# Optimization experiments

Hardware: AMD Instinct MI355X
Metric: run time of the kernel (lower is better)

Reference implementation:

```python
import jax, jax.numpy as jnp
import numpy as np

WS = 8          # window / grid size
HEADS = 4


def rel_pos_index(wh, ww):
    # Swin-style pairwise relative position index, [wh*ww, wh*ww]
    coords = np.stack(np.meshgrid(np.arange(wh), np.arange(ww), indexing='ij'))
    cf = coords.reshape(2, -1)
    rel = (cf[:, :, None] - cf[:, None, :]).transpose(1, 2, 0)
    rel[:, :, 0] += wh - 1
    rel[:, :, 1] += ww - 1
    rel[:, :, 0] *= 2 * ww - 1
    return rel.sum(-1)

REL_IDX = rel_pos_index(WS, WS)  # static, [N, N]


def setup_inputs() -> dict:
    key = jax.random.key(0)
    ks = jax.random.split(key, 8)
    B, C, H, W = 4, 128, 256, 256
    return {
        'x': jax.random.normal(ks[0], (B, C, H, W), jnp.float32),
        'w_qkv': jax.random.normal(ks[1], (C, 3 * C), jnp.float32) * 0.02,
        'b_qkv': jnp.zeros((3 * C,), jnp.float32),
        'w_proj': jax.random.normal(ks[2], (C, C), jnp.float32) * 0.02,
        'b_proj': jnp.zeros((C,), jnp.float32),
        'rpb_table': jax.random.normal(ks[3], ((2 * WS - 1) ** 2, HEADS), jnp.float32) * 0.02,
        'cf_w1': jax.random.normal(ks[4], (C, C), jnp.float32) * 0.02,
        'cf_w2': jax.random.normal(ks[5], (C, C), jnp.float32) * 0.02,
    }


def _window_partition(x):
    # [B,C,H,W] -> [B*nw, ws*ws, C], contiguous windows
    B, C, H, W = x.shape
    x = x.reshape(B, C, H // WS, WS, W // WS, WS)
    return x.transpose(0, 2, 4, 3, 5, 1).reshape(-1, WS * WS, C)


def _window_reverse(xw, B, C, H, W):
    x = xw.reshape(B, H // WS, W // WS, WS, WS, C)
    return x.transpose(0, 5, 1, 3, 2, 4).reshape(B, C, H, W)


def _grid_partition(x):
    # [B,C,H,W] -> [B*ng, gs*gs, C], strided (grid) windows
    B, C, H, W = x.shape
    x = x.reshape(B, C, WS, H // WS, WS, W // WS)
    return x.transpose(0, 3, 5, 2, 4, 1).reshape(-1, WS * WS, C)


def _grid_reverse(xg, B, C, H, W):
    x = xg.reshape(B, H // WS, W // WS, WS, WS, C)
    return x.transpose(0, 5, 3, 1, 4, 2).reshape(B, C, H, W)


def _rel_attention(xw, w_qkv, b_qkv, w_proj, b_proj, rpb_table):
    # xw: [Bw, N, C]  MaxViT-style relative self-attention
    Bw, N, C = xw.shape
    hd = C // HEADS
    qkv = (xw @ w_qkv + b_qkv).reshape(Bw, N, 3, HEADS, hd)
    q = qkv[:, :, 0].transpose(0, 2, 1, 3)  # [Bw,h,N,d]
    k = qkv[:, :, 1].transpose(0, 2, 1, 3)
    v = qkv[:, :, 2].transpose(0, 2, 1, 3)
    scale = HEADS ** -0.5
    bias = rpb_table[REL_IDX.reshape(-1)].reshape(N, N, HEADS).transpose(2, 0, 1)  # [h,N,N]
    logits = jnp.einsum('bhnd,bhmd->bhnm', q, k) * scale + bias[None]
    attn = jax.nn.softmax(logits, axis=-1)
    out = jnp.einsum('bhnm,bhmd->bhnd', attn, v)
    out = out.transpose(0, 2, 1, 3).reshape(Bw, N, C)
    return out @ w_proj + b_proj


def reference(x, w_qkv, b_qkv, w_proj, b_proj, rpb_table, cf_w1, cf_w2):
    B, C, H, W = x.shape
    # block (window) attention with residual
    xw = _window_partition(x)
    x = x + _window_reverse(_rel_attention(xw, w_qkv, b_qkv, w_proj, b_proj, rpb_table), B, C, H, W)
    # grid attention with residual
    xg = _grid_partition(x)
    x = x + _grid_reverse(_rel_attention(xg, w_qkv, b_qkv, w_proj, b_proj, rpb_table), B, C, H, W)
    # ChannelFocus: sigmoid(MLP(avgpool) + MLP(maxpool)) channel gate
    avg = x.mean(axis=(2, 3))  # [B,C]
    mx = x.max(axis=(2, 3))    # [B,C]
    mlp = lambda z: jax.nn.relu(z @ cf_w1) @ cf_w2
    gate = jax.nn.sigmoid(mlp(avg) + mlp(mx))  # [B,C]
    return x * gate[:, :, None, None]
```

## Files before the change

### kernel.cpp

```cpp
#include <hip/hip_runtime.h>
#include <hip/hip_bf16.h>
#include <stdint.h>

typedef __bf16 bf16;
typedef bf16 bf16x8 __attribute__((ext_vector_type(8)));
typedef bf16 bf16x4 __attribute__((ext_vector_type(4)));
typedef float f32x4 __attribute__((ext_vector_type(4)));

#define MFMA16(a, b, c) __builtin_amdgcn_mfma_f32_16x16x32_bf16((a), (b), (c), 0, 0, 0)
#define QKSWZ(n) ((((n) >> 2) & 3) << 3)
#define LGKM0() do { asm volatile("s_waitcnt lgkmcnt(0)" ::: "memory"); \
                     __builtin_amdgcn_sched_barrier(0); } while (0)

__global__ __launch_bounds__(256) void tin_kernel(const float* __restrict__ x,
                                                  bf16* __restrict__ xT)
{
    __shared__ float s[128 * 65];
    const int blk = blockIdx.x;
    const int b = blk >> 10;
    const int px0 = (blk & 1023) * 64;
    const int tid = threadIdx.x;
    {
        int c0 = tid >> 6, pxl = tid & 63;
        const float* src = x + (size_t)b * 8388608 + px0 + pxl;
#pragma unroll
        for (int i = 0; i < 32; ++i) {
            int c = c0 + i * 4;
            s[c * 65 + pxl] = src[(size_t)c * 65536];
        }
    }
    __syncthreads();
    int px = tid >> 2, piece = tid & 3;
    bf16* dstp = xT + ((size_t)b * 65536 + px0 + px) * 128;
#pragma unroll
    for (int k = 0; k < 4; ++k) {
        bf16x8 v8;
        int cb = (k * 4 + piece) * 8;
#pragma unroll
        for (int j = 0; j < 8; ++j) v8[j] = (bf16)s[(cb + j) * 65 + px];
        *(bf16x8*)(dstp + cb) = v8;
    }
}

__global__ void wconv_kernel(const float* __restrict__ w_qkv,
                             const float* __restrict__ w_proj,
                             bf16* __restrict__ wqkvT,
                             bf16* __restrict__ wprojT)
{
    int id = blockIdx.x * 256 + threadIdx.x;
    if (id < 49152) {
        int co = id >> 7, c = id & 127;
        wqkvT[id] = (bf16)w_qkv[c * 384 + co];
    } else {
        int id2 = id - 49152;
        int co = id2 >> 7, c = id2 & 127;
        wprojT[id2] = (bf16)w_proj[c * 128 + co];
    }
}

template<int STAGE>
__global__ __launch_bounds__(256, 3)
void attn_kernel(const bf16* __restrict__ xin, bf16* __restrict__ xout,
                 const bf16* __restrict__ wqkvT, const bf16* __restrict__ wprojT,
                 const float* __restrict__ b_qkv, const float* __restrict__ b_proj,
                 const float* __restrict__ rpb,
                 float* __restrict__ psum, float* __restrict__ pmax)
{
    __shared__ __align__(16) bf16 s_x[8192];
    __shared__ __align__(16) bf16 s_ex[8192];
    __shared__ bf16 s_rpb[904];

    const int tid = threadIdx.x;
    const int lane = tid & 63;
    const int wv = tid >> 6;
    const int lr = lane & 15;
    const int lg = lane >> 4;
    bf16* exq = s_ex + wv * 2048;
    bf16* exv = s_x + wv * 2048;

    const int blk = (blockIdx.x & 7) * 512 + (blockIdx.x >> 3);
    const int b  = blk >> 10;
    const int wr = (blk >> 5) & 31;
    const int wc = blk & 31;

    if constexpr (STAGE == 0) {
        int n = tid >> 2, piece = tid & 3;
        int ph = wr * 8 + (n >> 3), pw = wc * 8 + (n & 7);
        const bf16* src = xin + ((size_t)b * 65536 + (size_t)ph * 256 + pw) * 128;
#pragma unroll
        for (int k = 0; k < 4; ++k) {
            int cc = (k * 4 + piece) * 8;
            bf16x8 v = *(const bf16x8*)(src + cc);
            *(bf16x8*)&s_x[(n * 128 + cc) ^ ((n & 15) << 3)] = v;
        }
    } else {
        const bf16* src = xin + ((size_t)b * 65536 + (size_t)(wr * 32 + wc) * 64) * 128;
#pragma unroll
        for (int k = 0; k < 4; ++k) {
            int g = k * 256 + tid;
            int n = g >> 4, cc = (g & 15) * 8;
            bf16x8 v = *(const bf16x8*)(src + g * 8);
            *(bf16x8*)&s_x[(n * 128 + cc) ^ ((n & 15) << 3)] = v;
        }
    }
    for (int i = tid; i < 900; i += 256) s_rpb[i] = (bf16)rpb[i];

    __syncthreads();

    bf16x8 qb[4];
    {
        f32x4 acc[4][2];
#pragma unroll
        for (int mt = 0; mt < 4; ++mt)
#pragma unroll
            for (int t = 0; t < 2; ++t) acc[mt][t] = (f32x4){0.f, 0.f, 0.f, 0.f};
        bf16x8 wB[2][4];
#pragma unroll
        for (int t = 0; t < 2; ++t) {
            int co = wv * 32 + t * 16 + lr;
            const bf16* rp = wqkvT + co * 128 + lg * 8;
#pragma unroll
            for (int ks = 0; ks < 4; ++ks) wB[t][ks] = *(const bf16x8*)(rp + ks * 32);
        }
#pragma unroll
        for (int ks = 0; ks < 4; ++ks) {
            bf16x8 a[4];
#pragma unroll
            for (int mt = 0; mt < 4; ++mt) {
                int n = mt * 16 + lr;
                a[mt] = *(const bf16x8*)&s_x[(n * 128 + ks * 32 + lg * 8) ^ ((n & 15) << 3)];
            }
#pragma unroll
            for (int mt = 0; mt < 4; ++mt)
#pragma unroll
                for (int t = 0; t < 2; ++t)
                    acc[mt][t] = MFMA16(a[mt], wB[t][ks], acc[mt][t]);
        }
#pragma unroll
        for (int t = 0; t < 2; ++t) {
            float bias = b_qkv[wv * 32 + t * 16 + lr];
            int d = t * 16 + lr;
#pragma unroll
            for (int mt = 0; mt < 4; ++mt) {
                int n0 = mt * 16 + lg * 4;
#pragma unroll
                for (int r = 0; r < 4; ++r) {
                    int n = n0 + r;
                    exq[n * 32 + (d ^ QKSWZ(n))] = (bf16)(acc[mt][t][r] + bias);
                }
            }
        }
        LGKM0();
#pragma unroll
        for (int t = 0; t < 4; ++t) {
            int m = t * 16 + lr;
            qb[t] = *(const bf16x8*)&exq[m * 32 + ((lg * 8) ^ QKSWZ(m))];
        }
        LGKM0();
    }

    {
        f32x4 acc[4][2];
#pragma unroll
        for (int mt = 0; mt < 4; ++mt)
#pragma unroll
            for (int t = 0; t < 2; ++t) acc[mt][t] = (f32x4){0.f, 0.f, 0.f, 0.f};
        bf16x8 wB[2][4];
#pragma unroll
        for (int t = 0; t < 2; ++t) {
            int co = 128 + wv * 32 + t * 16 + lr;
            const bf16* rp = wqkvT + co * 128 + lg * 8;
#pragma unroll
            for (int ks = 0; ks < 4; ++ks) wB[t][ks] = *(const bf16x8*)(rp + ks * 32);
        }
#pragma unroll
        for (int ks = 0; ks < 4; ++ks) {
            bf16x8 a[4];
#pragma unroll
            for (int mt = 0; mt < 4; ++mt) {
                int n = mt * 16 + lr;
                a[mt] = *(const bf16x8*)&s_x[(n * 128 + ks * 32 + lg * 8) ^ ((n & 15) << 3)];
            }
#pragma unroll
            for (int mt = 0; mt < 4; ++mt)
#pragma unroll
                for (int t = 0; t < 2; ++t)
                    acc[mt][t] = MFMA16(a[mt], wB[t][ks], acc[mt][t]);
        }
#pragma unroll
        for (int t = 0; t < 2; ++t) {
            float bias = b_qkv[128 + wv * 32 + t * 16 + lr];
            int d = t * 16 + lr;
#pragma unroll
            for (int mt = 0; mt < 4; ++mt) {
                int n0 = mt * 16 + lg * 4;
#pragma unroll
                for (int r = 0; r < 4; ++r) {
                    int n = n0 + r;
                    exq[n * 32 + (d ^ QKSWZ(n))] = (bf16)(acc[mt][t][r] + bias);
                }
            }
        }
    }

    bf16x4 resr[2][4];
#pragma unroll
    for (int ct = 0; ct < 2; ++ct)
#pragma unroll
        for (int nt = 0; nt < 4; ++nt) {
            int n = nt * 16 + lr;
            int c0 = wv * 32 + ct * 16 + lg * 4;
            resr[ct][nt] = *(const bf16x4*)&s_x[(n * 128 + c0) ^ ((n & 15) << 3)];
        }

    f32x4 accV[4][2];
    {
#pragma unroll
        for (int mt = 0; mt < 4; ++mt)
#pragma unroll
            for (int t = 0; t < 2; ++t) accV[mt][t] = (f32x4){0.f, 0.f, 0.f, 0.f};
        bf16x8 wB[2][4];
#pragma unroll
        for (int t = 0; t < 2; ++t) {
            int co = 256 + wv * 32 + t * 16 + lr;
            const bf16* rp = wqkvT + co * 128 + lg * 8;
#pragma unroll
            for (int ks = 0; ks < 4; ++ks) wB[t][ks] = *(const bf16x8*)(rp + ks * 32);
        }
#pragma unroll
        for (int ks = 0; ks < 4; ++ks) {
            bf16x8 a[4];
#pragma unroll
            for (int mt = 0; mt < 4; ++mt) {
                int n = mt * 16 + lr;
                a[mt] = *(const bf16x8*)&s_x[(n * 128 + ks * 32 + lg * 8) ^ ((n & 15) << 3)];
            }
#pragma unroll
            for (int mt = 0; mt < 4; ++mt)
#pragma unroll
                for (int t = 0; t < 2; ++t)
                    accV[mt][t] = MFMA16(a[mt], wB[t][ks], accV[mt][t]);
        }
    }

    __syncthreads();

#pragma unroll
    for (int t = 0; t < 2; ++t) {
        float bias = b_qkv[256 + wv * 32 + t * 16 + lr];
        int d = t * 16 + lr;
#pragma unroll
        for (int mt = 0; mt < 4; ++mt) {
            bf16x4 v4;
#pragma unroll
            for (int r = 0; r < 4; ++r) v4[r] = (bf16)(accV[mt][t][r] + bias);
            int idx = (d * 64 + mt * 16 + lg * 4) ^ ((d & 7) << 3);
            *(bf16x4*)&exv[idx] = v4;
        }
    }

    f32x4 sacc[4][4];
#pragma unroll
    for (int mt = 0; mt < 4; ++mt)
#pragma unroll
        for (int nt = 0; nt < 4; ++nt) sacc[mt][nt] = (f32x4){0.f, 0.f, 0.f, 0.f};
#pragma unroll
    for (int mt = 0; mt < 4; ++mt) {
        int m = mt * 16 + lr;
        bf16x8 ka = *(const bf16x8*)&exq[m * 32 + ((lg * 8) ^ QKSWZ(m))];
#pragma unroll
        for (int nt = 0; nt < 4; ++nt)
            sacc[mt][nt] = MFMA16(ka, qb[nt], sacc[mt][nt]);
    }

    float inv[4];
#pragma unroll
    for (int nt = 0; nt < 4; ++nt) {
        int n = nt * 16 + lr;
        float mx = -1e30f;
#pragma unroll
        for (int mt = 0; mt < 4; ++mt)
#pragma unroll
            for (int r = 0; r < 4; ++r) {
                int m = mt * 16 + lg * 4 + r;
                int rel = ((n >> 3) - (m >> 3) + 7) * 15 + ((n & 7) - (m & 7) + 7);
                float lgt = sacc[mt][nt][r] * 0.5f + (float)s_rpb[rel * 4 + wv];
                sacc[mt][nt][r] = lgt;
                mx = fmaxf(mx, lgt);
            }
        mx = fmaxf(mx, __shfl_xor(mx, 16));
        mx = fmaxf(mx, __shfl_xor(mx, 32));
        float sum = 0.f;
#pragma unroll
        for (int mt = 0; mt < 4; ++mt)
#pragma unroll
            for (int r = 0; r < 4; ++r) {
                float p = __expf(sacc[mt][nt][r] - mx);
                sacc[mt][nt][r] = p;
                sum += p;
            }
        sum += __shfl_xor(sum, 16);
        sum += __shfl_xor(sum, 32);
        inv[nt] = 1.f / sum;
    }
    LGKM0();

    bf16x8 va[2][2];
#pragma unroll
    for (int dt = 0; dt < 2; ++dt) {
        int d = dt * 16 + lr;
#pragma unroll
        for (int ks = 0; ks < 2; ++ks)
            va[dt][ks] = *(const bf16x8*)&exv[(d * 64 + ks * 32 + lg * 8) ^ ((d & 7) << 3)];
    }

    __syncthreads();

    f32x4 oacc[2][4];
#pragma unroll
    for (int dt = 0; dt < 2; ++dt)
#pragma unroll
        for (int nt = 0; nt < 4; ++nt) oacc[dt][nt] = (f32x4){0.f, 0.f, 0.f, 0.f};
#pragma unroll
    for (int ks = 0; ks < 2; ++ks) {
#pragma unroll
        for (int nt = 0; nt < 4; ++nt) {
            int n = nt * 16 + lr;
#pragma unroll
            for (int mh = 0; mh < 2; ++mh) {
                int mt = ks * 2 + mh;
                bf16x4 v4;
#pragma unroll
                for (int r = 0; r < 4; ++r) v4[r] = (bf16)(sacc[mt][nt][r] * inv[nt]);
                int off = (mh * 16 + lg * 4) ^ ((n & 3) << 3);
                *(bf16x4*)&exq[n * 32 + off] = v4;
            }
        }
        LGKM0();
        bf16x8 pb[4];
#pragma unroll
        for (int nt = 0; nt < 4; ++nt) {
            int n = nt * 16 + lr;
            pb[nt] = *(const bf16x8*)&exq[n * 32 + ((lg * 8) ^ ((n & 3) << 3))];
        }
#pragma unroll
        for (int dt = 0; dt < 2; ++dt)
#pragma unroll
            for (int nt = 0; nt < 4; ++nt)
                oacc[dt][nt] = MFMA16(va[dt][ks], pb[nt], oacc[dt][nt]);
        LGKM0();
    }

#pragma unroll
    for (int dt = 0; dt < 2; ++dt)
#pragma unroll
        for (int nt = 0; nt < 4; ++nt) {
            int n = nt * 16 + lr;
            int c0 = wv * 32 + dt * 16 + lg * 4;
            bf16x4 v4;
#pragma unroll
            for (int r = 0; r < 4; ++r) v4[r] = (bf16)oacc[dt][nt][r];
            int idx = (n * 128 + c0) ^ ((n & 15) << 3);
            *(bf16x4*)&s_x[idx] = v4;
        }

    __syncthreads();

    f32x4 pacc[2][4];
#pragma unroll
    for (int ct = 0; ct < 2; ++ct)
#pragma unroll
        for (int nt = 0; nt < 4; ++nt) pacc[ct][nt] = (f32x4){0.f, 0.f, 0.f, 0.f};
#pragma unroll
    for (int ks = 0; ks < 4; ++ks) {
        bf16x8 wa[2], ab[4];
#pragma unroll
        for (int ct = 0; ct < 2; ++ct) {
            int co = wv * 32 + ct * 16 + lr;
            wa[ct] = *(const bf16x8*)(wprojT + co * 128 + ks * 32 + lg * 8);
        }
#pragma unroll
        for (int nt = 0; nt < 4; ++nt) {
            int n = nt * 16 + lr;
            ab[nt] = *(const bf16x8*)&s_x[(n * 128 + ks * 32 + lg * 8) ^ ((n & 15) << 3)];
        }
#pragma unroll
        for (int ct = 0; ct < 2; ++ct)
#pragma unroll
            for (int nt = 0; nt < 4; ++nt)
                pacc[ct][nt] = MFMA16(wa[ct], ab[nt], pacc[ct][nt]);
    }

    float bp[2][4];
#pragma unroll
    for (int ct = 0; ct < 2; ++ct)
#pragma unroll
        for (int r = 0; r < 4; ++r) bp[ct][r] = b_proj[wv * 32 + ct * 16 + lg * 4 + r];

    float vout[2][4][4];
    float ps[2][4], pm[2][4];
    if constexpr (STAGE == 1) {
#pragma unroll
        for (int ct = 0; ct < 2; ++ct)
#pragma unroll
            for (int r = 0; r < 4; ++r) { ps[ct][r] = 0.f; pm[ct][r] = -1e30f; }
    }
#pragma unroll
    for (int ct = 0; ct < 2; ++ct)
#pragma unroll
        for (int nt = 0; nt < 4; ++nt)
#pragma unroll
            for (int r = 0; r < 4; ++r) {
                float v = (float)resr[ct][nt][r] + bp[ct][r] + pacc[ct][nt][r];
                vout[ct][nt][r] = v;
                if constexpr (STAGE == 1) {
                    ps[ct][r] += v;
                    pm[ct][r] = fmaxf(pm[ct][r], v);
                }
            }

    if constexpr (STAGE == 1) {
        const int w = blk & 1023;
        float* prow_s = psum + (size_t)w * 512 + b * 128;
        float* prow_m = pmax + (size_t)w * 512 + b * 128;
#pragma unroll
        for (int ct = 0; ct < 2; ++ct)
#pragma unroll
            for (int r = 0; r < 4; ++r) {
                float s = ps[ct][r], m = pm[ct][r];
#pragma unroll
                for (int o = 1; o < 16; o <<= 1) {
                    s += __shfl_xor(s, o);
                    m = fmaxf(m, __shfl_xor(m, o));
                }
                if (lr == 0) {
                    int cout = wv * 32 + ct * 16 + lg * 4 + r;
                    prow_s[cout] = s;
                    prow_m[cout] = m;
                }
            }
    }

    __syncthreads();

#pragma unroll
    for (int ct = 0; ct < 2; ++ct)
#pragma unroll
        for (int nt = 0; nt < 4; ++nt) {
            int n = nt * 16 + lr;
            int c0 = wv * 32 + ct * 16 + lg * 4;
            bf16x4 o;
#pragma unroll
            for (int r = 0; r < 4; ++r) o[r] = (bf16)vout[ct][nt][r];
            *(bf16x4*)&s_x[(n * 128 + c0) ^ ((n & 15) << 3)] = o;
        }
    __syncthreads();

    if constexpr (STAGE == 0) {
        int px = tid >> 2, piece = tid & 3;
        int ph = wr * 8 + (px >> 3), pw = wc * 8 + (px & 7);
        int gw = ((ph & 31) << 5) + (pw & 31);
        int nn = ((ph >> 5) << 3) + (pw >> 5);
        bf16* drow = xout + ((size_t)b * 65536 + (size_t)gw * 64 + nn) * 128;
#pragma unroll
        for (int k = 0; k < 4; ++k) {
            int cc = (k * 4 + piece) * 8;
            *(bf16x8*)(drow + cc) =
                *(const bf16x8*)&s_x[(px * 128 + cc) ^ ((px & 15) << 3)];
        }
    } else {
        bf16* dst = xout + ((size_t)b * 65536 + (size_t)(wr * 32 + wc) * 64) * 128;
#pragma unroll
        for (int k = 0; k < 4; ++k) {
            int g = k * 256 + tid;
            int n = g >> 4, cc = (g & 15) * 8;
            *(bf16x8*)(dst + g * 8) =
                *(const bf16x8*)&s_x[(n * 128 + cc) ^ ((n & 15) << 3)];
        }
    }
}

__global__ __launch_bounds__(64) void reduce_kernel(const float* __restrict__ psum,
                                                    const float* __restrict__ pmax,
                                                    float* __restrict__ avg,
                                                    float* __restrict__ mx)
{
    int bc = blockIdx.x;
    int t = threadIdx.x;
    float s = 0.f, m = -1e30f;
#pragma unroll
    for (int k = 0; k < 16; ++k) {
        size_t w = t + k * 64;
        s += psum[w * 512 + bc];
        m = fmaxf(m, pmax[w * 512 + bc]);
    }
#pragma unroll
    for (int o = 1; o < 64; o <<= 1) {
        s += __shfl_xor(s, o);
        m = fmaxf(m, __shfl_xor(m, o));
    }
    if (t == 0) { avg[bc] = s * (1.f / 65536.f); mx[bc] = m; }
}

__global__ void gate_kernel(const float* __restrict__ avg, const float* __restrict__ mxp,
                            const float* __restrict__ w1, const float* __restrict__ w2,
                            float* __restrict__ gate)
{
    __shared__ float la[512], lm[512], s1[512];
    int t = threadIdx.x;
    la[t] = avg[t];
    lm[t] = mxp[t];
    __syncthreads();
    int b = t >> 7, co = t & 127;
    float a1 = 0.f, m1 = 0.f;
    for (int c = 0; c < 128; ++c) {
        float w = w1[c * 128 + co];
        a1 += la[b * 128 + c] * w;
        m1 += lm[b * 128 + c] * w;
    }
    s1[t] = fmaxf(a1, 0.f) + fmaxf(m1, 0.f);
    __syncthreads();
    float g = 0.f;
    for (int c = 0; c < 128; ++c) g += s1[b * 128 + c] * w2[c * 128 + co];
    gate[t] = 1.f / (1.f + __expf(-g));
}

__global__ __launch_bounds__(256) void tout_kernel(const bf16* __restrict__ x2,
                                                   const float* __restrict__ gate,
                                                   float* __restrict__ out)
{
    __shared__ float s[128 * 68];
    __shared__ float sg[128];
    const int blk = blockIdx.x;
    const int b = blk >> 10;
    const int chunk = blk & 1023;
    const int ph = chunk >> 2, pw0 = (chunk & 3) * 64;
    const int gwb = (ph & 31) << 5;
    const int nb  = ((ph >> 5) << 3) + (pw0 >> 5);
    const int t = threadIdx.x;
    if (t < 128) sg[t] = gate[b * 128 + t];
    __syncthreads();
    const bf16* base = x2 + (size_t)b * 65536 * 128;
#pragma unroll
    for (int i = 0; i < 4; ++i) {
        int idx8 = t + i * 256;
        int px = idx8 >> 4, c8 = idx8 & 15;
        size_t pi = (size_t)(gwb + (px & 31)) * 64 + nb + (px >> 5);
        bf16x8 v = *(const bf16x8*)(base + pi * 128 + c8 * 8);
        int pxs = px ^ ((c8 & 7) << 3);
#pragma unroll
        for (int j = 0; j < 8; ++j) {
            int c = c8 * 8 + j;
            s[c * 68 + pxs] = (float)v[j] * sg[c];
        }
    }
    __syncthreads();
    int cg = t >> 4, pl = (t & 15) * 4;
#pragma unroll
    for (int i = 0; i < 8; ++i) {
        int c = cg + i * 16;
        int pp = pl ^ (((c >> 3) & 7) << 3);
        f32x4 w = *(const f32x4*)&s[c * 68 + pp];
        *(f32x4*)&out[((size_t)(b * 128 + c)) * 65536 + ph * 256 + pw0 + pl] = w;
    }
}

extern "C" void kernel_launch(void* const* d_in, const int* in_sizes, int n_in,
                              void* d_out, int out_size, void* d_ws, size_t ws_size,
                              hipStream_t stream)
{
    const float* x      = (const float*)d_in[0];
    const float* w_qkv  = (const float*)d_in[1];
    const float* b_qkv  = (const float*)d_in[2];
    const float* w_proj = (const float*)d_in[3];
    const float* b_proj = (const float*)d_in[4];
    const float* rpb    = (const float*)d_in[5];
    const float* cf_w1  = (const float*)d_in[6];
    const float* cf_w2  = (const float*)d_in[7];
    float* out = (float*)d_out;

    char* ws = (char*)d_ws;
    bf16* xT = (bf16*)ws;
    bf16* x2 = (bf16*)ws;
    char* tail = ws + 67108864;
    bf16*  wqkvT  = (bf16*)tail;
    bf16*  wprojT = (bf16*)(tail + 98304);
    float* psum   = (float*)(tail + 131072);
    float* pmax   = (float*)(tail + 131072 + 2097152);
    float* avg    = (float*)(tail + 131072 + 4194304);
    float* mxp    = (float*)(tail + 131072 + 4196352);
    float* gate   = (float*)(tail + 131072 + 4198400);
    bf16*  x1T    = (bf16*)d_out;

    tin_kernel<<<4096, 256, 0, stream>>>(x, xT);
    wconv_kernel<<<256, 256, 0, stream>>>(w_qkv, w_proj, wqkvT, wprojT);
    attn_kernel<0><<<4096, 256, 0, stream>>>(xT,  x1T, wqkvT, wprojT,
                                             b_qkv, b_proj, rpb, nullptr, nullptr);
    attn_kernel<1><<<4096, 256, 0, stream>>>(x1T, x2,  wqkvT, wprojT,
                                             b_qkv, b_proj, rpb, psum, pmax);
    reduce_kernel<<<512, 64, 0, stream>>>(psum, pmax, avg, mxp);
    gate_kernel<<<1, 512, 0, stream>>>(avg, mxp, cf_w1, cf_w2, gate);
    tout_kernel<<<4096, 256, 0, stream>>>(x2, gate, out);
}
```

Measured before the change: 311.4 us.

## Pack two windows per block, store outputs directly, move bias table to global

Each attention block now handles two windows with 512 threads, each half using its own shared buffers. The relative position bias table is converted to bf16 once in the weight-conversion kernel and read from global memory instead of being staged per block. The epilogue writes results straight from registers to global memory as 8-byte stores, dropping the shared-memory round trip and two barriers. The cost is narrower, less coalesced global stores, scattered bias loads from global or cache, and different register pressure under the new launch bounds.

```diff
diff --git a/kernel.cpp b/kernel.cpp
--- a/kernel.cpp
+++ b/kernel.cpp
@@ -44,10 +44,13 @@
 
 __global__ void wconv_kernel(const float* __restrict__ w_qkv,
                              const float* __restrict__ w_proj,
+                             const float* __restrict__ rpb,
                              bf16* __restrict__ wqkvT,
-                             bf16* __restrict__ wprojT)
+                             bf16* __restrict__ wprojT,
+                             bf16* __restrict__ rpbh)
 {
     int id = blockIdx.x * 256 + threadIdx.x;
+    if (id < 900) rpbh[id] = (bf16)rpb[id];
     if (id < 49152) {
         int co = id >> 7, c = id & 127;
         wqkvT[id] = (bf16)w_qkv[c * 384 + co];
@@ -59,32 +62,35 @@
 }
 
 template<int STAGE>
-__global__ __launch_bounds__(256, 3)
+__global__ __launch_bounds__(512, 2)
 void attn_kernel(const bf16* __restrict__ xin, bf16* __restrict__ xout,
                  const bf16* __restrict__ wqkvT, const bf16* __restrict__ wprojT,
                  const float* __restrict__ b_qkv, const float* __restrict__ b_proj,
-                 const float* __restrict__ rpb,
+                 const bf16* __restrict__ rpbh,
                  float* __restrict__ psum, float* __restrict__ pmax)
 {
-    __shared__ __align__(16) bf16 s_x[8192];
-    __shared__ __align__(16) bf16 s_ex[8192];
-    __shared__ bf16 s_rpb[904];
+    __shared__ __align__(16) bf16 s_xs[2][8192];
+    __shared__ __align__(16) bf16 s_exs[2][8192];
 
     const int tid = threadIdx.x;
+    const int win = tid >> 8;
+    const int tl  = tid & 255;
     const int lane = tid & 63;
-    const int wv = tid >> 6;
+    const int wv = (tid >> 6) & 3;
     const int lr = lane & 15;
     const int lg = lane >> 4;
-    bf16* exq = s_ex + wv * 2048;
+    bf16* s_x = s_xs[win];
+    bf16* exq = s_exs[win] + wv * 2048;
     bf16* exv = s_x + wv * 2048;
 
-    const int blk = (blockIdx.x & 7) * 512 + (blockIdx.x >> 3);
-    const int b  = blk >> 10;
-    const int wr = (blk >> 5) & 31;
-    const int wc = blk & 31;
+    const int pr = (blockIdx.x & 7) * 256 + (blockIdx.x >> 3);
+    const int wid = pr * 2 + win;
+    const int b  = wid >> 10;
+    const int wr = (wid >> 5) & 31;
+    const int wc = wid & 31;
 
     if constexpr (STAGE == 0) {
-        int n = tid >> 2, piece = tid & 3;
+        int n = tl >> 2, piece = tl & 3;
         int ph = wr * 8 + (n >> 3), pw = wc * 8 + (n & 7);
         const bf16* src = xin + ((size_t)b * 65536 + (size_t)ph * 256 + pw) * 128;
 #pragma unroll
@@ -97,13 +103,12 @@
         const bf16* src = xin + ((size_t)b * 65536 + (size_t)(wr * 32 + wc) * 64) * 128;
 #pragma unroll
         for (int k = 0; k < 4; ++k) {
-            int g = k * 256 + tid;
+            int g = k * 256 + tl;
             int n = g >> 4, cc = (g & 15) * 8;
             bf16x8 v = *(const bf16x8*)(src + g * 8);
             *(bf16x8*)&s_x[(n * 128 + cc) ^ ((n & 15) << 3)] = v;
         }
     }
-    for (int i = tid; i < 900; i += 256) s_rpb[i] = (bf16)rpb[i];
 
     __syncthreads();
 
@@ -284,7 +289,7 @@
             for (int r = 0; r < 4; ++r) {
                 int m = mt * 16 + lg * 4 + r;
                 int rel = ((n >> 3) - (m >> 3) + 7) * 15 + ((n & 7) - (m & 7) + 7);
-                float lgt = sacc[mt][nt][r] * 0.5f + (float)s_rpb[rel * 4 + wv];
+                float lgt = sacc[mt][nt][r] * 0.5f + (float)rpbh[rel * 4 + wv];
                 sacc[mt][nt][r] = lgt;
                 mx = fmaxf(mx, lgt);
             }
@@ -397,7 +402,6 @@
 #pragma unroll
         for (int r = 0; r < 4; ++r) bp[ct][r] = b_proj[wv * 32 + ct * 16 + lg * 4 + r];
 
-    float vout[2][4][4];
     float ps[2][4], pm[2][4];
     if constexpr (STAGE == 1) {
 #pragma unroll
@@ -405,22 +409,37 @@
 #pragma unroll
             for (int r = 0; r < 4; ++r) { ps[ct][r] = 0.f; pm[ct][r] = -1e30f; }
     }
+
 #pragma unroll
     for (int ct = 0; ct < 2; ++ct)
 #pragma unroll
-        for (int nt = 0; nt < 4; ++nt)
+        for (int nt = 0; nt < 4; ++nt) {
+            int n = nt * 16 + lr;
+            int c0 = wv * 32 + ct * 16 + lg * 4;
+            bf16x4 o;
 #pragma unroll
             for (int r = 0; r < 4; ++r) {
                 float v = (float)resr[ct][nt][r] + bp[ct][r] + pacc[ct][nt][r];
-                vout[ct][nt][r] = v;
+                o[r] = (bf16)v;
                 if constexpr (STAGE == 1) {
                     ps[ct][r] += v;
                     pm[ct][r] = fmaxf(pm[ct][r], v);
                 }
             }
+            size_t pix;
+            if constexpr (STAGE == 0) {
+                int ph = wr * 8 + (n >> 3), pw = wc * 8 + (n & 7);
+                int gw = ((ph & 31) << 5) + (pw & 31);
+                int nn = ((ph >> 5) << 3) + (pw >> 5);
+                pix = (size_t)b * 65536 + (size_t)gw * 64 + nn;
+            } else {
+                pix = (size_t)b * 65536 + (size_t)(wr * 32 + wc) * 64 + n;
+            }
+            *(bf16x4*)(xout + pix * 128 + c0) = o;
+        }
 
     if constexpr (STAGE == 1) {
-        const int w = blk & 1023;
+        const int w = wid & 1023;
         float* prow_s = psum + (size_t)w * 512 + b * 128;
         float* prow_m = pmax + (size_t)w * 512 + b * 128;
 #pragma unroll
@@ -439,44 +458,6 @@
                     prow_m[cout] = m;
                 }
             }
-    }
-
-    __syncthreads();
-
-#pragma unroll
-    for (int ct = 0; ct < 2; ++ct)
-#pragma unroll
-        for (int nt = 0; nt < 4; ++nt) {
-            int n = nt * 16 + lr;
-            int c0 = wv * 32 + ct * 16 + lg * 4;
-            bf16x4 o;
-#pragma unroll
-            for (int r = 0; r < 4; ++r) o[r] = (bf16)vout[ct][nt][r];
-            *(bf16x4*)&s_x[(n * 128 + c0) ^ ((n & 15) << 3)] = o;
-        }
-    __syncthreads();
-
-    if constexpr (STAGE == 0) {
-        int px = tid >> 2, piece = tid & 3;
-        int ph = wr * 8 + (px >> 3), pw = wc * 8 + (px & 7);
-        int gw = ((ph & 31) << 5) + (pw & 31);
-        int nn = ((ph >> 5) << 3) + (pw >> 5);
-        bf16* drow = xout + ((size_t)b * 65536 + (size_t)gw * 64 + nn) * 128;
-#pragma unroll
-        for (int k = 0; k < 4; ++k) {
-            int cc = (k * 4 + piece) * 8;
-            *(bf16x8*)(drow + cc) =
-                *(const bf16x8*)&s_x[(px * 128 + cc) ^ ((px & 15) << 3)];
-        }
-    } else {
-        bf16* dst = xout + ((size_t)b * 65536 + (size_t)(wr * 32 + wc) * 64) * 128;
-#pragma unroll
-        for (int k = 0; k < 4; ++k) {
-            int g = k * 256 + tid;
-            int n = g >> 4, cc = (g & 15) * 8;
-            *(bf16x8*)(dst + g * 8) =
-                *(const bf16x8*)&s_x[(n * 128 + cc) ^ ((n & 15) << 3)];
-        }
     }
 }
 
@@ -590,14 +571,15 @@
     float* avg    = (float*)(tail + 131072 + 4194304);
     float* mxp    = (float*)(tail + 131072 + 4196352);
     float* gate   = (float*)(tail + 131072 + 4198400);
+    bf16*  rpbh   = (bf16*)(tail + 131072 + 4200448);
     bf16*  x1T    = (bf16*)d_out;
 
     tin_kernel<<<4096, 256, 0, stream>>>(x, xT);
-    wconv_kernel<<<256, 256, 0, stream>>>(w_qkv, w_proj, wqkvT, wprojT);
-    attn_kernel<0><<<4096, 256, 0, stream>>>(xT,  x1T, wqkvT, wprojT,
-                                             b_qkv, b_proj, rpb, nullptr, nullptr);
-    attn_kernel<1><<<4096, 256, 0, stream>>>(x1T, x2,  wqkvT, wprojT,
-                                             b_qkv, b_proj, rpb, psum, pmax);
+    wconv_kernel<<<256, 256, 0, stream>>>(w_qkv, w_proj, rpb, wqkvT, wprojT, rpbh);
+    attn_kernel<0><<<2048, 512, 0, stream>>>(xT,  x1T, wqkvT, wprojT,
+                                             b_qkv, b_proj, rpbh, nullptr, nullptr);
+    attn_kernel<1><<<2048, 512, 0, stream>>>(x1T, x2,  wqkvT, wprojT,
+                                             b_qkv, b_proj, rpbh, psum, pmax);
     reduce_kernel<<<512, 64, 0, stream>>>(psum, pmax, avg, mxp);
     gate_kernel<<<1, 512, 0, stream>>>(avg, mxp, cf_w1, cf_w2, gate);
     tout_kernel<<<4096, 256, 0, stream>>>(x2, gate, out);
```

Result: slower. 413.4 us (+32.7%).
